# Kernel tuning notes

Measured on AMD Instinct MI355X. Metric: run time of the kernel, lower is better.

The kernel has to match this reference:

```python
import jax, jax.numpy as jnp
import numpy as np

B, H, S, D = 4, 8, 8192, 128
HALF = D // 2            # 64
ROPE = 64                # rope_retained_dim
NOPE = D - ROPE          # 64
RANK = 512
IN_FEAT = NOPE * H + D * H  # 1536


def setup_inputs() -> dict:
    key = jax.random.key(0)
    k1, k2, k3, k4, k5 = jax.random.split(key, 5)
    return {
        "K_evicted": jax.random.normal(k1, (B, H, S, D), dtype=jnp.float32),
        "V_evicted": jax.random.normal(k2, (B, H, S, D), dtype=jnp.float32),
        "U_l": jax.random.normal(k3, (HALF, HALF), dtype=jnp.float32) / np.sqrt(HALF),
        "R_KV": jax.random.normal(k4, (IN_FEAT, RANK), dtype=jnp.float32) / np.sqrt(IN_FEAT),
        "alpha": jax.random.uniform(k5, (1,), dtype=jnp.float32) + 0.5,
    }


def reference(K_evicted, V_evicted, U_l, R_KV, alpha):
    b, h, s, d = K_evicted.shape
    half = d // 2
    # [b, s, h, d]
    K_perm = jnp.transpose(K_evicted, (0, 2, 1, 3))
    K_x = K_perm[..., :half]
    K_y = K_perm[..., half:]
    # rotate each half by U_l: x @ U_l.T
    K_x_rot = jnp.einsum('bshd,ed->bshe', K_x, U_l)
    K_y_rot = jnp.einsum('bshd,ed->bshe', K_y, U_l)
    K_rotated = jnp.concatenate([K_x_rot, K_y_rot], axis=-1)  # [b,s,h,d]
    K_rope = K_rotated[..., :ROPE]                            # [b,s,h,ROPE]
    K_nope = K_rotated[..., ROPE:] / alpha                    # [b,s,h,NOPE]
    K_nope_flat = K_nope.reshape(b, s, -1)                    # [b,s,h*NOPE]
    V_flat = jnp.transpose(V_evicted, (0, 2, 1, 3)).reshape(b, s, -1)  # [b,s,h*d]
    C_nope = jnp.concatenate([K_nope_flat, V_flat], axis=-1)  # [b,s,IN_FEAT]
    C_kv = C_nope @ R_KV                                      # [b,s,RANK]
    K_rope = jnp.transpose(K_rope, (0, 2, 1, 3))              # [b,h,s,ROPE]
    return C_kv, K_rope
```

## Files before the change

### kernel.cpp

```cpp
#include <hip/hip_runtime.h>
#include <hip/hip_bf16.h>

#define B_    4
#define H_    8
#define S_    8192
#define D_    128
#define RANK_ 512
#define KTOT  1536
#define MTOT  32768
#define NROWS (B_*H_*S_)
#define C_ELEMS (MTOT*RANK_)

typedef __attribute__((ext_vector_type(4))) float  f32x4;
typedef __attribute__((ext_vector_type(8))) short  short8;

static __device__ __forceinline__ short f2bf(float f) {
  union { __hip_bfloat16 h; short s; } u;
  u.h = __float2bfloat16(f);
  return u.s;
}

static __device__ __forceinline__ void gload_lds16(const void* gsrc, void* ldst) {
  __builtin_amdgcn_global_load_lds(
      (const __attribute__((address_space(1))) void*)gsrc,
      (__attribute__((address_space(3))) void*)ldst, 16, 0, 0);
}

__global__ __launch_bounds__(256) void build_b_kernel(
    const float* __restrict__ U, const float* __restrict__ R,
    const float* __restrict__ alpha, short* __restrict__ wsB)
{
  const int j0 = blockIdx.x * 8;
  const int t  = threadIdx.x;
  float vals[2][8];

  if (j0 < 512) {
    const int h   = j0 >> 6;
    const int dy0 = j0 & 63;
    const float ia = 1.0f / alpha[0];
    float acc0[8], acc1[8];
#pragma unroll
    for (int kk = 0; kk < 8; ++kk) { acc0[kk] = 0.f; acc1[kk] = 0.f; }
    for (int e = 0; e < 64; ++e) {
      const float r0 = R[(h*64 + e)*RANK_ + t];
      const float r1 = R[(h*64 + e)*RANK_ + t + 256];
#pragma unroll
      for (int kk = 0; kk < 8; ++kk) {
        const float u = U[e*64 + dy0 + kk];
        acc0[kk] += u * r0;
        acc1[kk] += u * r1;
      }
    }
#pragma unroll
    for (int kk = 0; kk < 8; ++kk) {
      vals[0][kk] = acc0[kk] * ia;
      vals[1][kk] = acc1[kk] * ia;
    }
  } else {
#pragma unroll
    for (int kk = 0; kk < 8; ++kk) {
      vals[0][kk] = R[(size_t)(j0 + kk)*RANK_ + t];
      vals[1][kk] = R[(size_t)(j0 + kk)*RANK_ + t + 256];
    }
  }

  const int kb = j0 >> 6;
  const int c  = (j0 >> 3) & 7;
  char* base = (char*)wsB + (size_t)kb*65536 + (size_t)c*8192;
#pragma unroll
  for (int half = 0; half < 2; ++half) {
    const int r = t + half*256;
    short8 o;
#pragma unroll
    for (int kk = 0; kk < 8; ++kk) o[kk] = f2bf(vals[half][kk]);
    *(short8*)(base + (size_t)r*16) = o;
  }
}

__global__ __launch_bounds__(256) void rope_kernel(
    const float* __restrict__ K, const float* __restrict__ U,
    float* __restrict__ Orope)
{
  __shared__ float ks[4][64];
  const int lane = threadIdx.x & 63;
  const int wid  = threadIdx.x >> 6;

  float4 u4[16];
#pragma unroll
  for (int i = 0; i < 16; ++i)
    u4[i] = *(const float4*)&U[lane*64 + i*4];

  const int gw = blockIdx.x*4 + wid;
  const int nw = gridDim.x*4;
  for (int row = gw; row < NROWS; row += nw) {
    const float kx = K[(size_t)row*D_ + lane];
    ks[wid][lane] = kx;
    float acc = 0.f;
#pragma unroll
    for (int i = 0; i < 16; ++i) {
      const float4 kk = *(const float4*)&ks[wid][i*4];
      acc += kk.x*u4[i].x + kk.y*u4[i].y + kk.z*u4[i].z + kk.w*u4[i].w;
    }
    Orope[(size_t)row*64 + lane] = acc;
  }
}

__global__ __launch_bounds__(512, 2) void gemm_kernel(
    const float* __restrict__ Kp, const float* __restrict__ Vp,
    const short* __restrict__ wsB, float* __restrict__ C)
{
  __shared__ short A_lds[8*128*8];
  __shared__ short B_lds[8*512*8];

  const int tid  = threadIdx.x;
  const int lane = tid & 63;
  const int wid  = tid >> 6;
  const int wave_m = wid >> 2;
  const int wave_n = wid & 3;
  const int row0 = blockIdx.x * 128;

  const int r = tid >> 2;
  const int q = tid & 3;
  const int m_stage = row0 + r;
  const int b = m_stage >> 13;
  const int s = m_stage & 8191;
  const size_t rowbase = ((size_t)(b*H_))*S_*D_ + (size_t)s*D_;

  const int am   = wave_m*64  + (lane & 15);
  const int bn   = wave_n*128 + (lane & 15);
  const int kblk = lane >> 4;

  f32x4 acc[4][8];
#pragma unroll
  for (int mi = 0; mi < 4; ++mi)
#pragma unroll
    for (int ni = 0; ni < 8; ++ni)
      acc[mi][ni] = (f32x4){0.f, 0.f, 0.f, 0.f};

  for (int kb = 0; kb < 24; ++kb) {
    {
      const char* gsrc = (const char*)wsB + (size_t)kb*65536 + wid*8192 + lane*16;
      char*       ldst = (char*)B_lds     +                  wid*8192 + lane*16;
#pragma unroll
      for (int i = 0; i < 8; ++i)
        gload_lds16(gsrc + i*1024, ldst + i*1024);
    }
    {
      const int j0 = kb*64;
      const float* asrc;
      if (j0 < 512) {
        const int h = j0 >> 6;
        asrc = Kp + rowbase + (size_t)h*S_*D_ + 64;
      } else {
        const int jj = j0 - 512;
        const int h  = jj >> 7;
        asrc = Vp + rowbase + (size_t)h*S_*D_ + (jj & 127);
      }
      const float* tsrc = asrc + q*16;
      const float4 l0 = *(const float4*)(tsrc +  0);
      const float4 l1 = *(const float4*)(tsrc +  4);
      const float4 l2 = *(const float4*)(tsrc +  8);
      const float4 l3 = *(const float4*)(tsrc + 12);
      short8 c0, c1;
      c0[0]=f2bf(l0.x); c0[1]=f2bf(l0.y); c0[2]=f2bf(l0.z); c0[3]=f2bf(l0.w);
      c0[4]=f2bf(l1.x); c0[5]=f2bf(l1.y); c0[6]=f2bf(l1.z); c0[7]=f2bf(l1.w);
      c1[0]=f2bf(l2.x); c1[1]=f2bf(l2.y); c1[2]=f2bf(l2.z); c1[3]=f2bf(l2.w);
      c1[4]=f2bf(l3.x); c1[5]=f2bf(l3.y); c1[6]=f2bf(l3.z); c1[7]=f2bf(l3.w);
      *(short8*)((char*)A_lds + (size_t)(2*q  )*2048 + (size_t)r*16) = c0;
      *(short8*)((char*)A_lds + (size_t)(2*q+1)*2048 + (size_t)r*16) = c1;
    }
    __syncthreads();

#pragma unroll
    for (int ks = 0; ks < 2; ++ks) {
      const int cA = ks*4 + kblk;
      short8 af[4], bfr[8];
#pragma unroll
      for (int mi = 0; mi < 4; ++mi)
        af[mi] = *(const short8*)((const char*)A_lds + cA*2048 + (size_t)(am + mi*16)*16);
#pragma unroll
      for (int ni = 0; ni < 8; ++ni)
        bfr[ni] = *(const short8*)((const char*)B_lds + cA*8192 + (size_t)(bn + ni*16)*16);
#pragma unroll
      for (int mi = 0; mi < 4; ++mi)
#pragma unroll
        for (int ni = 0; ni < 8; ++ni)
          acc[mi][ni] = __builtin_amdgcn_mfma_f32_16x16x32_bf16(
              af[mi], bfr[ni], acc[mi][ni], 0, 0, 0);
    }
    __syncthreads();
  }

  const int erow = (lane >> 4)*4;
#pragma unroll
  for (int mi = 0; mi < 4; ++mi)
#pragma unroll
    for (int ni = 0; ni < 8; ++ni)
#pragma unroll
      for (int rg = 0; rg < 4; ++rg) {
        const int row = row0 + wave_m*64 + mi*16 + erow + rg;
        const int col = wave_n*128 + ni*16 + (lane & 15);
        C[(size_t)row*RANK_ + col] = acc[mi][ni][rg];
      }
}

extern "C" void kernel_launch(void* const* d_in, const int* in_sizes, int n_in,
                              void* d_out, int out_size, void* d_ws, size_t ws_size,
                              hipStream_t stream) {
  const float* K     = (const float*)d_in[0];
  const float* V     = (const float*)d_in[1];
  const float* U     = (const float*)d_in[2];
  const float* R     = (const float*)d_in[3];
  const float* alpha = (const float*)d_in[4];
  float* C     = (float*)d_out;
  float* Orope = (float*)d_out + C_ELEMS;
  short* wsB   = (short*)d_ws;

  build_b_kernel<<<192,  256, 0, stream>>>(U, R, alpha, wsB);
  rope_kernel   <<<2048, 256, 0, stream>>>(K, U, Orope);
  gemm_kernel   <<<256,  512, 0, stream>>>(K, V, wsB, C);
}
```

Measured before the change: 403.3 us.

## Double-buffer B tiles and prefetch A into registers in GEMM; pair rows in rope

```diff
diff --git a/kernel.cpp b/kernel.cpp
--- a/kernel.cpp
+++ b/kernel.cpp
@@ -6,7 +6,6 @@
 #define S_    8192
 #define D_    128
 #define RANK_ 512
-#define KTOT  1536
 #define MTOT  32768
 #define NROWS (B_*H_*S_)
 #define C_ELEMS (MTOT*RANK_)
@@ -81,7 +80,7 @@
     const float* __restrict__ K, const float* __restrict__ U,
     float* __restrict__ Orope)
 {
-  __shared__ float ks[4][64];
+  __shared__ float ks[4][2][64];
   const int lane = threadIdx.x & 63;
   const int wid  = threadIdx.x >> 6;
 
@@ -92,16 +91,22 @@
 
   const int gw = blockIdx.x*4 + wid;
   const int nw = gridDim.x*4;
-  for (int row = gw; row < NROWS; row += nw) {
-    const float kx = K[(size_t)row*D_ + lane];
-    ks[wid][lane] = kx;
-    float acc = 0.f;
+  for (int pair = gw; pair < NROWS/2; pair += nw) {
+    const int row0 = pair*2;
+    const float k0 = K[(size_t)row0*D_ + lane];
+    const float k1 = K[(size_t)row0*D_ + D_ + lane];
+    ks[wid][0][lane] = k0;
+    ks[wid][1][lane] = k1;
+    float a0 = 0.f, a1 = 0.f;
 #pragma unroll
     for (int i = 0; i < 16; ++i) {
-      const float4 kk = *(const float4*)&ks[wid][i*4];
-      acc += kk.x*u4[i].x + kk.y*u4[i].y + kk.z*u4[i].z + kk.w*u4[i].w;
-    }
-    Orope[(size_t)row*64 + lane] = acc;
+      const float4 c0 = *(const float4*)&ks[wid][0][i*4];
+      const float4 c1 = *(const float4*)&ks[wid][1][i*4];
+      a0 += c0.x*u4[i].x + c0.y*u4[i].y + c0.z*u4[i].z + c0.w*u4[i].w;
+      a1 += c1.x*u4[i].x + c1.y*u4[i].y + c1.z*u4[i].z + c1.w*u4[i].w;
+    }
+    Orope[(size_t)row0*64 + lane]      = a0;
+    Orope[(size_t)row0*64 + 64 + lane] = a1;
   }
 }
 
@@ -109,8 +114,8 @@
     const float* __restrict__ Kp, const float* __restrict__ Vp,
     const short* __restrict__ wsB, float* __restrict__ C)
 {
+  __shared__ short B_lds[2][8*512*8];
   __shared__ short A_lds[8*128*8];
-  __shared__ short B_lds[8*512*8];
 
   const int tid  = threadIdx.x;
   const int lane = tid & 63;
@@ -137,40 +142,51 @@
     for (int ni = 0; ni < 8; ++ni)
       acc[mi][ni] = (f32x4){0.f, 0.f, 0.f, 0.f};
 
+  f32x4 st[4];
+
+  auto issueA = [&](int kb) {
+    const float* asrc;
+    if (kb < 8) {
+      asrc = Kp + rowbase + (size_t)kb*S_*D_ + 64;
+    } else {
+      const int jj = (kb - 8) * 64;
+      asrc = Vp + rowbase + (size_t)(jj >> 7)*S_*D_ + (jj & 127);
+    }
+    const float* tsrc = asrc + q*16;
+    st[0] = *(const f32x4*)(tsrc +  0);
+    st[1] = *(const f32x4*)(tsrc +  4);
+    st[2] = *(const f32x4*)(tsrc +  8);
+    st[3] = *(const f32x4*)(tsrc + 12);
+  };
+
+  auto writeA = [&]() {
+    short8 c0, c1;
+#pragma unroll
+    for (int i = 0; i < 4; ++i) { c0[i]   = f2bf(st[0][i]); c0[4+i] = f2bf(st[1][i]); }
+#pragma unroll
+    for (int i = 0; i < 4; ++i) { c1[i]   = f2bf(st[2][i]); c1[4+i] = f2bf(st[3][i]); }
+    *(short8*)((char*)A_lds + (size_t)(2*q  )*2048 + (size_t)r*16) = c0;
+    *(short8*)((char*)A_lds + (size_t)(2*q+1)*2048 + (size_t)r*16) = c1;
+  };
+
+  auto issueB = [&](int t) {
+    const char* gsrc = (const char*)wsB + (size_t)t*65536 + wid*8192 + lane*16;
+    char*       ldst = (char*)B_lds[t & 1]               + wid*8192 + lane*16;
+#pragma unroll
+    for (int i = 0; i < 8; ++i)
+      gload_lds16(gsrc + i*1024, ldst + i*1024);
+  };
+
+  issueB(0);
+  issueB(1);
+  issueA(0);
+  writeA();
+  __syncthreads();
+
   for (int kb = 0; kb < 24; ++kb) {
-    {
-      const char* gsrc = (const char*)wsB + (size_t)kb*65536 + wid*8192 + lane*16;
-      char*       ldst = (char*)B_lds     +                  wid*8192 + lane*16;
-#pragma unroll
-      for (int i = 0; i < 8; ++i)
-        gload_lds16(gsrc + i*1024, ldst + i*1024);
-    }
-    {
-      const int j0 = kb*64;
-      const float* asrc;
-      if (j0 < 512) {
-        const int h = j0 >> 6;
-        asrc = Kp + rowbase + (size_t)h*S_*D_ + 64;
-      } else {
-        const int jj = j0 - 512;
-        const int h  = jj >> 7;
-        asrc = Vp + rowbase + (size_t)h*S_*D_ + (jj & 127);
-      }
-      const float* tsrc = asrc + q*16;
-      const float4 l0 = *(const float4*)(tsrc +  0);
-      const float4 l1 = *(const float4*)(tsrc +  4);
-      const float4 l2 = *(const float4*)(tsrc +  8);
-      const float4 l3 = *(const float4*)(tsrc + 12);
-      short8 c0, c1;
-      c0[0]=f2bf(l0.x); c0[1]=f2bf(l0.y); c0[2]=f2bf(l0.z); c0[3]=f2bf(l0.w);
-      c0[4]=f2bf(l1.x); c0[5]=f2bf(l1.y); c0[6]=f2bf(l1.z); c0[7]=f2bf(l1.w);
-      c1[0]=f2bf(l2.x); c1[1]=f2bf(l2.y); c1[2]=f2bf(l2.z); c1[3]=f2bf(l2.w);
-      c1[4]=f2bf(l3.x); c1[5]=f2bf(l3.y); c1[6]=f2bf(l3.z); c1[7]=f2bf(l3.w);
-      *(short8*)((char*)A_lds + (size_t)(2*q  )*2048 + (size_t)r*16) = c0;
-      *(short8*)((char*)A_lds + (size_t)(2*q+1)*2048 + (size_t)r*16) = c1;
-    }
-    __syncthreads();
-
+    if (kb + 1 < 24) issueA(kb + 1);
+
+    const short* Bcur = B_lds[kb & 1];
 #pragma unroll
     for (int ks = 0; ks < 2; ++ks) {
       const int cA = ks*4 + kblk;
@@ -180,7 +196,7 @@
         af[mi] = *(const short8*)((const char*)A_lds + cA*2048 + (size_t)(am + mi*16)*16);
 #pragma unroll
       for (int ni = 0; ni < 8; ++ni)
-        bfr[ni] = *(const short8*)((const char*)B_lds + cA*8192 + (size_t)(bn + ni*16)*16);
+        bfr[ni] = *(const short8*)((const char*)Bcur + cA*8192 + (size_t)(bn + ni*16)*16);
 #pragma unroll
       for (int mi = 0; mi < 4; ++mi)
 #pragma unroll
@@ -188,7 +204,16 @@
           acc[mi][ni] = __builtin_amdgcn_mfma_f32_16x16x32_bf16(
               af[mi], bfr[ni], acc[mi][ni], 0, 0, 0);
     }
-    __syncthreads();
+
+    if (kb + 1 < 24) {
+      __syncthreads();
+      if (kb + 2 < 24) issueB(kb + 2);
+      writeA();
+      asm volatile("s_waitcnt lgkmcnt(0)" ::: "memory");
+      __builtin_amdgcn_sched_barrier(0);
+      __builtin_amdgcn_s_barrier();
+      __builtin_amdgcn_sched_barrier(0);
+    }
   }
 
   const int erow = (lane >> 4)*4;
@@ -212,11 +237,11 @@
   const float* U     = (const float*)d_in[2];
   const float* R     = (const float*)d_in[3];
   const float* alpha = (const float*)d_in[4];
-  float* C     = (float*)d_out;
+  float* Cv    = (float*)d_out;
   float* Orope = (float*)d_out + C_ELEMS;
   short* wsB   = (short*)d_ws;
 
   build_b_kernel<<<192,  256, 0, stream>>>(U, R, alpha, wsB);
   rope_kernel   <<<2048, 256, 0, stream>>>(K, U, Orope);
-  gemm_kernel   <<<256,  512, 0, stream>>>(K, V, wsB, C);
-}
+  gemm_kernel   <<<256,  512, 0, stream>>>(K, V, wsB, Cv);
+}
```

Measured after the change: 381.6 us. 5.4% less time.
